# Kernel optimization log

Measured on AMD Instinct MI355X. Metric: run time of the kernel, lower is better.

Reference implementation:

```python
import jax, jax.numpy as jnp
import numpy as np

IN_F, HID, OUT = 128, 128, 32
N_NODES, N_EDGES, N_GRAPHS = 100000, 1600000, 64


def gcn_conv(x, W, b, src, dst, n):
    """PyG-style GCNConv: add self-loops, symmetric deg^-1/2 norm, linear, scatter-add."""
    h = x @ W  # [N, F_out]
    loop = jnp.arange(n)
    src_f = jnp.concatenate([src, loop])
    dst_f = jnp.concatenate([dst, loop])
    deg = jax.ops.segment_sum(jnp.ones_like(dst_f, dtype=x.dtype), dst_f, num_segments=n)
    dinv = jax.lax.rsqrt(jnp.maximum(deg, 1.0))  # deg >= 1 because of self-loops
    norm = dinv[src_f] * dinv[dst_f]             # [E+N]
    msg = h[src_f] * norm[:, None]               # gather + scale, [E+N, F_out]
    out = jax.ops.segment_sum(msg, dst_f, num_segments=n)  # scatter-add
    return out + b


def setup_inputs() -> dict:
    key = jax.random.key(0)
    ks = jax.random.split(key, 10)
    x = jax.random.normal(ks[0], (N_NODES, IN_F), dtype=jnp.float32)
    edge_index = jax.random.randint(ks[1], (2, N_EDGES), 0, N_NODES, dtype=jnp.int64)
    batch = jnp.sort(jax.random.randint(ks[2], (N_NODES,), 0, N_GRAPHS, dtype=jnp.int64))

    def glorot(k, fi, fo):
        s = np.sqrt(6.0 / (fi + fo)).astype(np.float32)
        return jax.random.uniform(k, (fi, fo), dtype=jnp.float32, minval=-s, maxval=s)

    return {
        "x": x,
        "edge_index": edge_index,
        "batch": batch,
        "num_graphs": N_GRAPHS,
        "W1": glorot(ks[3], IN_F, HID), "b1": jnp.zeros((HID,), jnp.float32),
        "W2": glorot(ks[4], HID, HID), "b2": jnp.zeros((HID,), jnp.float32),
        "W3": glorot(ks[5], HID, OUT), "b3": jnp.zeros((OUT,), jnp.float32),
    }


def reference(x, edge_index, batch, num_graphs, W1, b1, W2, b2, W3, b3):
    n = x.shape[0]
    src, dst = edge_index[0], edge_index[1]
    # Dropout is identity in eval mode.
    h = jax.nn.relu(gcn_conv(x, W1, b1, src, dst, n))
    h = jax.nn.relu(gcn_conv(h, W2, b2, src, dst, n))
    h = gcn_conv(h, W3, b3, src, dst, n)  # [N, OUT]
    # global_mean_pool over batch ids
    sums = jax.ops.segment_sum(h, batch, num_segments=num_graphs)
    cnts = jax.ops.segment_sum(jnp.ones((n,), h.dtype), batch, num_segments=num_graphs)
    x_global = sums / jnp.maximum(cnts, 1.0)[:, None]
    return h, x_global
```

## Files before the change

kernel.cpp:

```cpp
#include <hip/hip_runtime.h>
#include <hip/hip_bf16.h>


typedef unsigned int uint32;
typedef short short8 __attribute__((ext_vector_type(8)));
typedef float f32x4 __attribute__((ext_vector_type(4)));

static __device__ __forceinline__ unsigned short f2bf(float f) {
    uint32 u = __float_as_uint(f);
    return (unsigned short)((u + 0x7fffu + ((u >> 16) & 1u)) >> 16);
}
static __device__ __forceinline__ float bf2f_lo(uint32 u) {
    return __uint_as_float(u << 16);
}
static __device__ __forceinline__ float bf2f_hi(uint32 u) {
    return __uint_as_float(u & 0xffff0000u);
}

__global__ __launch_bounds__(256) void initdeg_k(int* deg, int M) {
    int i = blockIdx.x * 256 + threadIdx.x;
    if (i < M) deg[i] = 1;
}

__global__ __launch_bounds__(256) void count_k(const int* __restrict__ dst, int E,
                                               int* __restrict__ deg) {
    int e = blockIdx.x * 256 + threadIdx.x;
    if (e < E) atomicAdd(&deg[dst[e]], 1);
}

__global__ __launch_bounds__(256) void mkdinv_k(const int* __restrict__ deg,
                                                float* __restrict__ dinv, int M) {
    int i = blockIdx.x * 256 + threadIdx.x;
    if (i < M) dinv[i] = rsqrtf((float)deg[i]);
}

__global__ __launch_bounds__(256) void scan1_k(const int* __restrict__ deg, int M,
                                               int* __restrict__ blksum) {
    __shared__ int sh[256];
    int i = blockIdx.x * 256 + threadIdx.x;
    int v = (i < M) ? deg[i] - 1 : 0;
    sh[threadIdx.x] = v;
    __syncthreads();
    for (int o = 128; o > 0; o >>= 1) {
        if (threadIdx.x < o) sh[threadIdx.x] += sh[threadIdx.x + o];
        __syncthreads();
    }
    if (threadIdx.x == 0) blksum[blockIdx.x] = sh[0];
}

__global__ __launch_bounds__(512) void scan2_k(int* __restrict__ blksum, int nb) {
    __shared__ int sh[512];
    int tid = threadIdx.x;
    int v = (tid < nb) ? blksum[tid] : 0;
    sh[tid] = v;
    __syncthreads();
    for (int o = 1; o < 512; o <<= 1) {
        int t = (tid >= o) ? sh[tid - o] : 0;
        __syncthreads();
        sh[tid] += t;
        __syncthreads();
    }
    if (tid < nb) blksum[tid] = sh[tid] - v;
}

__global__ __launch_bounds__(256) void scan3_k(const int* __restrict__ deg, int M,
                                               const int* __restrict__ blksum,
                                               int* __restrict__ rowptr,
                                               int* __restrict__ cursor) {
    __shared__ int sh[256];
    int tid = threadIdx.x;
    int i = blockIdx.x * 256 + tid;
    int v = (i < M) ? deg[i] - 1 : 0;
    sh[tid] = v;
    __syncthreads();
    for (int o = 1; o < 256; o <<= 1) {
        int t = (tid >= o) ? sh[tid - o] : 0;
        __syncthreads();
        sh[tid] += t;
        __syncthreads();
    }
    int excl = sh[tid] - v + blksum[blockIdx.x];
    if (i < M) {
        rowptr[i] = excl;
        cursor[i] = excl;
    }
    if (i == M - 1) rowptr[M] = excl + v;
}

#define FILL_CHUNK 4096
__global__ __launch_bounds__(256) void fill_rp_k(const int* __restrict__ src,
                                                 const int* __restrict__ dst,
                                                 int E, int M,
                                                 int* __restrict__ cursor,
                                                 int* __restrict__ col) {
    const int r = blockIdx.x & 7;
    const int chunk = blockIdx.x >> 3;
    const int lo = (int)(((long long)r * M) >> 3);
    const int hi = (int)(((long long)(r + 1) * M) >> 3);
    const int base = chunk * FILL_CHUNK;
    const int end = min(E, base + FILL_CHUNK);
    for (int e = base + (int)threadIdx.x; e < end; e += 256) {
        int d = dst[e];
        int s = src[e];
        if (d >= lo && d < hi) {
            int slot = atomicAdd(&cursor[d], 1);
            col[slot] = s;
        }
    }
}

__global__ __launch_bounds__(256) void cvt_k(const float* __restrict__ x,
                                             unsigned short* __restrict__ o,
                                             int n8) {
    int i = blockIdx.x * 256 + threadIdx.x;
    if (i >= n8) return;
    const float4* xp = (const float4*)x + (size_t)i * 2;
    float4 a = xp[0], b = xp[1];
    union { unsigned short us[8]; uint4 v; } u;
    u.us[0] = f2bf(a.x); u.us[1] = f2bf(a.y); u.us[2] = f2bf(a.z); u.us[3] = f2bf(a.w);
    u.us[4] = f2bf(b.x); u.us[5] = f2bf(b.y); u.us[6] = f2bf(b.z); u.us[7] = f2bf(b.w);
    *((uint4*)o + i) = u.v;
}

__global__ __launch_bounds__(256) void wt_k(const float* __restrict__ W,
                                            unsigned short* __restrict__ Wt,
                                            int N) {
    int idx = blockIdx.x * 256 + threadIdx.x;
    if (idx >= N * 128) return;
    int n = idx >> 7, k = idx & 127;
    Wt[idx] = f2bf(W[k * N + n]);
}

template <int NT>
__global__ __launch_bounds__(256) void mgemm_k(const unsigned short* __restrict__ A,
                                               const unsigned short* __restrict__ Wt,
                                               unsigned short* __restrict__ C,
                                               int M, int nstrips) {
    constexpr int N = NT * 16;
    const int lane = threadIdx.x & 63;
    const int wid = threadIdx.x >> 6;
    const int r = lane & 15;
    const int g = lane >> 4;

    short8 wf[NT][4];
#pragma unroll
    for (int t = 0; t < NT; t++)
#pragma unroll
        for (int s = 0; s < 4; s++)
            wf[t][s] = *(const short8*)&Wt[(size_t)(t * 16 + r) * 128 + s * 32 + g * 8];

    const int stride = gridDim.x * 4;
    for (int strip = blockIdx.x * 4 + wid; strip < nstrips; strip += stride) {
        const int R = strip * 16;
        const int ar = min(R + r, M - 1);
        short8 af[4];
#pragma unroll
        for (int s = 0; s < 4; s++)
            af[s] = *(const short8*)&A[(size_t)ar * 128 + s * 32 + g * 8];
        f32x4 acc[NT];
#pragma unroll
        for (int t = 0; t < NT; t++) acc[t] = (f32x4){0.f, 0.f, 0.f, 0.f};
#pragma unroll
        for (int s = 0; s < 4; s++)
#pragma unroll
            for (int t = 0; t < NT; t++)
                acc[t] = __builtin_amdgcn_mfma_f32_16x16x32_bf16(
                    af[s], wf[t][s], acc[t], 0, 0, 0);
#pragma unroll
        for (int j = 0; j < 4; j++) {
            int row = R + 4 * g + j;
            if (row < M) {
#pragma unroll
                for (int t = 0; t < NT; t++)
                    C[(size_t)row * N + t * 16 + r] = f2bf(acc[t][j]);
            }
        }
    }
}

__global__ __launch_bounds__(256) void agg128_k(const unsigned short* __restrict__ Hb,
                                                const int* __restrict__ rowptr,
                                                const int* __restrict__ col,
                                                const float* __restrict__ dinv,
                                                const float* __restrict__ bias,
                                                unsigned short* __restrict__ outb,
                                                int M, int relu) {
    int node = blockIdx.x * 4 + (threadIdx.x >> 6);
    if (node >= M) return;
    int lane = threadIdx.x & 63;
    const float di = dinv[node];
    const uint32* Hu = (const uint32*)Hb;
    uint32 su = Hu[(size_t)node * 64 + lane];
    float ax = di * di * bf2f_lo(su);
    float ay = di * di * bf2f_hi(su);
    const int s = rowptr[node], e = rowptr[node + 1];

    for (int base = s; base < e; base += 64) {
        int n = e - base;
        if (n > 64) n = 64;
        int cid = col[base + (lane < n ? lane : 0)];
        float w = di * dinv[cid];
        int j = 0;
        for (; j + 8 <= n; j += 8) {
            int sj[8]; float wj[8]; uint32 u[8];
#pragma unroll
            for (int k = 0; k < 8; k++) {
                sj[k] = __shfl(cid, j + k);
                wj[k] = __shfl(w, j + k);
            }
#pragma unroll
            for (int k = 0; k < 8; k++)
                u[k] = Hu[(size_t)sj[k] * 64 + lane];
#pragma unroll
            for (int k = 0; k < 8; k++) {
                ax = fmaf(wj[k], bf2f_lo(u[k]), ax);
                ay = fmaf(wj[k], bf2f_hi(u[k]), ay);
            }
        }
        for (; j < n; j++) {
            int s0 = __shfl(cid, j);
            float w0 = __shfl(w, j);
            uint32 u0 = Hu[(size_t)s0 * 64 + lane];
            ax = fmaf(w0, bf2f_lo(u0), ax);
            ay = fmaf(w0, bf2f_hi(u0), ay);
        }
    }
    float2 bv = *(const float2*)&bias[lane * 2];
    float ox = ax + bv.x, oy = ay + bv.y;
    if (relu) { ox = fmaxf(ox, 0.f); oy = fmaxf(oy, 0.f); }
    uint32 pk = (uint32)f2bf(ox) | ((uint32)f2bf(oy) << 16);
    *(uint32*)&outb[(size_t)node * 128 + lane * 2] = pk;
}

__global__ __launch_bounds__(256) void agg32_k(const unsigned short* __restrict__ Hb,
                                               const int* __restrict__ rowptr,
                                               const int* __restrict__ col,
                                               const float* __restrict__ dinv,
                                               const float* __restrict__ bias,
                                               float* __restrict__ out, int M) {
    int node = blockIdx.x * 4 + (threadIdx.x >> 6);
    if (node >= M) return;
    int lane = threadIdx.x & 63;
    int f = lane & 31;
    int half = lane >> 5;
    const float di = dinv[node];
    float acc = 0.f;
    if (!half)
        acc = di * di * __uint_as_float(((uint32)Hb[(size_t)node * 32 + f]) << 16);
    const int s = rowptr[node], e = rowptr[node + 1];
    int i = s + half;
    for (; i + 6 < e; i += 8) {
        int s0 = col[i], s1 = col[i + 2], s2 = col[i + 4], s3 = col[i + 6];
        float w0 = di * dinv[s0], w1 = di * dinv[s1];
        float w2 = di * dinv[s2], w3 = di * dinv[s3];
        float h0 = __uint_as_float(((uint32)Hb[(size_t)s0 * 32 + f]) << 16);
        float h1 = __uint_as_float(((uint32)Hb[(size_t)s1 * 32 + f]) << 16);
        float h2 = __uint_as_float(((uint32)Hb[(size_t)s2 * 32 + f]) << 16);
        float h3 = __uint_as_float(((uint32)Hb[(size_t)s3 * 32 + f]) << 16);
        acc = fmaf(w0, h0, acc);
        acc = fmaf(w1, h1, acc);
        acc = fmaf(w2, h2, acc);
        acc = fmaf(w3, h3, acc);
    }
    for (; i < e; i += 2) {
        int s0 = col[i];
        float h0 = __uint_as_float(((uint32)Hb[(size_t)s0 * 32 + f]) << 16);
        acc = fmaf(di * dinv[s0], h0, acc);
    }
    acc += __shfl_xor(acc, 32);
    if (!half) out[(size_t)node * 32 + f] = acc + bias[f];
}

__global__ __launch_bounds__(256) void pool_k(const float* __restrict__ h,
                                              const int* __restrict__ batch, int M,
                                              float* __restrict__ out) {
    int g = blockIdx.x;
    int lo, hi;
    {
        int l = 0, r = M;
        while (l < r) { int m = (l + r) >> 1; if (batch[m] < g) l = m + 1; else r = m; }
        lo = l;
    }
    {
        int l = lo, r = M;
        while (l < r) { int m = (l + r) >> 1; if (batch[m] < g + 1) l = m + 1; else r = m; }
        hi = l;
    }
    int f = threadIdx.x & 31;
    int chunk = threadIdx.x >> 5;
    float acc = 0.f;
    for (int i = lo + chunk; i < hi; i += 8) acc += h[(size_t)i * 32 + f];
    __shared__ float red[8][32];
    red[chunk][f] = acc;
    __syncthreads();
    if (threadIdx.x < 32) {
        float s = 0.f;
#pragma unroll
        for (int c = 0; c < 8; c++) s += red[c][f];
        out[g * 32 + f] = s / fmaxf((float)(hi - lo), 1.f);
    }
}

extern "C" void kernel_launch(void* const* d_in, const int* in_sizes, int n_in,
                              void* d_out, int out_size, void* d_ws, size_t ws_size,
                              hipStream_t stream) {
    const float* x   = (const float*)d_in[0];
    const int* ei    = (const int*)d_in[1];
    const int* batch = (const int*)d_in[2];
    const float* W1  = (const float*)d_in[4];
    const float* b1  = (const float*)d_in[5];
    const float* W2  = (const float*)d_in[6];
    const float* b2  = (const float*)d_in[7];
    const float* W3  = (const float*)d_in[8];
    const float* b3  = (const float*)d_in[9];

    const int M = in_sizes[0] / 128;
    const int E = in_sizes[1] / 2;
    const int G = 64;
    const int* srcp = ei;
    const int* dstp = ei + E;

    char* p = (char*)d_ws;
    auto carve = [&](size_t bytes) {
        void* r = (void*)p;
        p += (bytes + 255) & ~(size_t)255;
        return r;
    };
    int*   deg    = (int*)carve((size_t)M * 4);
    float* dinv   = (float*)carve((size_t)M * 4);
    int*   rowptr = (int*)carve((size_t)(M + 1) * 4);
    int*   cursor = (int*)carve((size_t)M * 4);
    int*   blksum = (int*)carve(512 * 4);
    int*   col    = (int*)carve((size_t)E * 4);
    unsigned short* Xb = (unsigned short*)carve((size_t)M * 128 * 2);
    unsigned short* Hb = (unsigned short*)carve((size_t)M * 128 * 2);
    unsigned short* Ob = (unsigned short*)carve((size_t)M * 128 * 2);
    unsigned short* Wt1 = (unsigned short*)carve(128 * 128 * 2);
    unsigned short* Wt2 = (unsigned short*)carve(128 * 128 * 2);
    unsigned short* Wt3 = (unsigned short*)carve(32 * 128 * 2);

    float* outh = (float*)d_out;
    float* outg = outh + (size_t)M * 32;

    const int nbM = (M + 255) / 256;
    const int nbE = (E + 255) / 256;
    const int nstrips = (M + 15) / 16;
    const int gblk = (nstrips + 7) / 8;

    cvt_k<<<(M * 128 / 8 + 255) / 256, 256, 0, stream>>>(x, Xb, M * 128 / 8);
    initdeg_k<<<nbM, 256, 0, stream>>>(deg, M);
    count_k<<<nbE, 256, 0, stream>>>(dstp, E, deg);
    mkdinv_k<<<nbM, 256, 0, stream>>>(deg, dinv, M);
    scan1_k<<<nbM, 256, 0, stream>>>(deg, M, blksum);
    scan2_k<<<1, 512, 0, stream>>>(blksum, nbM);
    scan3_k<<<nbM, 256, 0, stream>>>(deg, M, blksum, rowptr, cursor);
    {
        const int nchunk = (E + FILL_CHUNK - 1) / FILL_CHUNK;
        fill_rp_k<<<nchunk * 8, 256, 0, stream>>>(srcp, dstp, E, M, cursor, col);
    }
    wt_k<<<(128 * 128 + 255) / 256, 256, 0, stream>>>(W1, Wt1, 128);
    wt_k<<<(128 * 128 + 255) / 256, 256, 0, stream>>>(W2, Wt2, 128);
    wt_k<<<(32 * 128 + 255) / 256, 256, 0, stream>>>(W3, Wt3, 32);

    mgemm_k<8><<<gblk, 256, 0, stream>>>(Xb, Wt1, Hb, M, nstrips);
    agg128_k<<<(M + 3) / 4, 256, 0, stream>>>(Hb, rowptr, col, dinv, b1, Ob, M, 1);
    mgemm_k<8><<<gblk, 256, 0, stream>>>(Ob, Wt2, Hb, M, nstrips);
    agg128_k<<<(M + 3) / 4, 256, 0, stream>>>(Hb, rowptr, col, dinv, b2, Ob, M, 1);
    mgemm_k<2><<<gblk, 256, 0, stream>>>(Ob, Wt3, Hb, M, nstrips);
    agg32_k<<<(M + 3) / 4, 256, 0, stream>>>(Hb, rowptr, col, dinv, b3, outh, M);
    pool_k<<<G, 256, 0, stream>>>(outh, batch, M, outg);
}
```

Baseline: 570.2 us.

## Slice feature layout into 16-wide planes and fold source norm into GEMM

Stores node features as eight 16-column slices (slice-major), so each aggregation block works on one 32-byte slice across many nodes, shrinking the gathered working set per pass for better cache reuse. The source-side deg^-1/2 factor is folded into the GEMM epilogue, which removes the per-edge dinv gather and multiply from the aggregation; the destination factor is applied once per node at the end. Nontemporal hints are added to the streaming edge and column loads. Because gathers become 32-byte rows per slice, sector efficiency depends on how the L2 cache handles the eight slice passes.

```diff
diff --git a/kernel.cpp b/kernel.cpp
--- a/kernel.cpp
+++ b/kernel.cpp
@@ -25,7 +25,7 @@
 __global__ __launch_bounds__(256) void count_k(const int* __restrict__ dst, int E,
                                                int* __restrict__ deg) {
     int e = blockIdx.x * 256 + threadIdx.x;
-    if (e < E) atomicAdd(&deg[dst[e]], 1);
+    if (e < E) atomicAdd(&deg[__builtin_nontemporal_load(&dst[e])], 1);
 }
 
 __global__ __launch_bounds__(256) void mkdinv_k(const int* __restrict__ deg,
@@ -100,8 +100,8 @@
     const int base = chunk * FILL_CHUNK;
     const int end = min(E, base + FILL_CHUNK);
     for (int e = base + (int)threadIdx.x; e < end; e += 256) {
-        int d = dst[e];
-        int s = src[e];
+        int d = __builtin_nontemporal_load(&dst[e]);
+        int s = __builtin_nontemporal_load(&src[e]);
         if (d >= lo && d < hi) {
             int slot = atomicAdd(&cursor[d], 1);
             col[slot] = s;
@@ -111,7 +111,7 @@
 
 __global__ __launch_bounds__(256) void cvt_k(const float* __restrict__ x,
                                              unsigned short* __restrict__ o,
-                                             int n8) {
+                                             int M, int n8) {
     int i = blockIdx.x * 256 + threadIdx.x;
     if (i >= n8) return;
     const float4* xp = (const float4*)x + (size_t)i * 2;
@@ -119,7 +119,10 @@
     union { unsigned short us[8]; uint4 v; } u;
     u.us[0] = f2bf(a.x); u.us[1] = f2bf(a.y); u.us[2] = f2bf(a.z); u.us[3] = f2bf(a.w);
     u.us[4] = f2bf(b.x); u.us[5] = f2bf(b.y); u.us[6] = f2bf(b.z); u.us[7] = f2bf(b.w);
-    *((uint4*)o + i) = u.v;
+    int node = i >> 4;
+    int k0 = (i & 15) * 8;
+    size_t di = ((size_t)(k0 >> 4) * M + node) * 16 + (k0 & 15);
+    *(uint4*)&o[di] = u.v;
 }
 
 __global__ __launch_bounds__(256) void wt_k(const float* __restrict__ W,
@@ -131,9 +134,10 @@
     Wt[idx] = f2bf(W[k * N + n]);
 }
 
-template <int NT>
+template <int NT, bool SOUT>
 __global__ __launch_bounds__(256) void mgemm_k(const unsigned short* __restrict__ A,
                                                const unsigned short* __restrict__ Wt,
+                                               const float* __restrict__ dinv,
                                                unsigned short* __restrict__ C,
                                                int M, int nstrips) {
     constexpr int N = NT * 16;
@@ -155,8 +159,10 @@
         const int ar = min(R + r, M - 1);
         short8 af[4];
 #pragma unroll
-        for (int s = 0; s < 4; s++)
-            af[s] = *(const short8*)&A[(size_t)ar * 128 + s * 32 + g * 8];
+        for (int s = 0; s < 4; s++) {
+            const int q = 2 * s + (g >> 1);
+            af[s] = *(const short8*)&A[((size_t)q * M + ar) * 16 + (g & 1) * 8];
+        }
         f32x4 acc[NT];
 #pragma unroll
         for (int t = 0; t < NT; t++) acc[t] = (f32x4){0.f, 0.f, 0.f, 0.f};
@@ -170,66 +176,70 @@
         for (int j = 0; j < 4; j++) {
             int row = R + 4 * g + j;
             if (row < M) {
-#pragma unroll
-                for (int t = 0; t < NT; t++)
-                    C[(size_t)row * N + t * 16 + r] = f2bf(acc[t][j]);
+                float dv = dinv[row];
+#pragma unroll
+                for (int t = 0; t < NT; t++) {
+                    unsigned short v = f2bf(dv * acc[t][j]);
+                    if (SOUT)
+                        C[((size_t)t * M + row) * 16 + r] = v;
+                    else
+                        C[(size_t)row * N + t * 16 + r] = v;
+                }
             }
         }
     }
 }
 
-__global__ __launch_bounds__(256) void agg128_k(const unsigned short* __restrict__ Hb,
-                                                const int* __restrict__ rowptr,
-                                                const int* __restrict__ col,
-                                                const float* __restrict__ dinv,
-                                                const float* __restrict__ bias,
-                                                unsigned short* __restrict__ outb,
-                                                int M, int relu) {
-    int node = blockIdx.x * 4 + (threadIdx.x >> 6);
+__global__ __launch_bounds__(256) void agg128s_k(const unsigned short* __restrict__ Hs,
+                                                 const int* __restrict__ rowptr,
+                                                 const int* __restrict__ col,
+                                                 const float* __restrict__ dinv,
+                                                 const float* __restrict__ bias,
+                                                 unsigned short* __restrict__ Os,
+                                                 int M, int relu) {
+    const int slice = blockIdx.x & 7;
+    const int nb = blockIdx.x >> 3;
+    const int lane = threadIdx.x & 63;
+    const int wid = threadIdx.x >> 6;
+    const int grp = lane >> 3;
+    const int j = lane & 7;
+    const int node = nb * 32 + wid * 8 + grp;
     if (node >= M) return;
-    int lane = threadIdx.x & 63;
-    const float di = dinv[node];
-    const uint32* Hu = (const uint32*)Hb;
-    uint32 su = Hu[(size_t)node * 64 + lane];
-    float ax = di * di * bf2f_lo(su);
-    float ay = di * di * bf2f_hi(su);
+    const uint32* H = (const uint32*)Hs + (size_t)slice * M * 8;
+    uint32* O = (uint32*)Os + (size_t)slice * M * 8;
+
+    float a0, a1;
+    {
+        uint32 u = H[(size_t)node * 8 + j];
+        a0 = bf2f_lo(u); a1 = bf2f_hi(u);
+    }
     const int s = rowptr[node], e = rowptr[node + 1];
-
-    for (int base = s; base < e; base += 64) {
-        int n = e - base;
-        if (n > 64) n = 64;
-        int cid = col[base + (lane < n ? lane : 0)];
-        float w = di * dinv[cid];
-        int j = 0;
-        for (; j + 8 <= n; j += 8) {
-            int sj[8]; float wj[8]; uint32 u[8];
-#pragma unroll
-            for (int k = 0; k < 8; k++) {
-                sj[k] = __shfl(cid, j + k);
-                wj[k] = __shfl(w, j + k);
-            }
-#pragma unroll
-            for (int k = 0; k < 8; k++)
-                u[k] = Hu[(size_t)sj[k] * 64 + lane];
-#pragma unroll
-            for (int k = 0; k < 8; k++) {
-                ax = fmaf(wj[k], bf2f_lo(u[k]), ax);
-                ay = fmaf(wj[k], bf2f_hi(u[k]), ay);
-            }
-        }
-        for (; j < n; j++) {
-            int s0 = __shfl(cid, j);
-            float w0 = __shfl(w, j);
-            uint32 u0 = Hu[(size_t)s0 * 64 + lane];
-            ax = fmaf(w0, bf2f_lo(u0), ax);
-            ay = fmaf(w0, bf2f_hi(u0), ay);
-        }
-    }
-    float2 bv = *(const float2*)&bias[lane * 2];
-    float ox = ax + bv.x, oy = ay + bv.y;
+    int i = s;
+    for (; i + 4 <= e; i += 4) {
+        int c0 = __builtin_nontemporal_load(&col[i]);
+        int c1 = __builtin_nontemporal_load(&col[i + 1]);
+        int c2 = __builtin_nontemporal_load(&col[i + 2]);
+        int c3 = __builtin_nontemporal_load(&col[i + 3]);
+        uint32 u0 = H[(size_t)c0 * 8 + j];
+        uint32 u1 = H[(size_t)c1 * 8 + j];
+        uint32 u2 = H[(size_t)c2 * 8 + j];
+        uint32 u3 = H[(size_t)c3 * 8 + j];
+        a0 += bf2f_lo(u0); a1 += bf2f_hi(u0);
+        a0 += bf2f_lo(u1); a1 += bf2f_hi(u1);
+        a0 += bf2f_lo(u2); a1 += bf2f_hi(u2);
+        a0 += bf2f_lo(u3); a1 += bf2f_hi(u3);
+    }
+    for (; i < e; i++) {
+        int c0 = __builtin_nontemporal_load(&col[i]);
+        uint32 u0 = H[(size_t)c0 * 8 + j];
+        a0 += bf2f_lo(u0); a1 += bf2f_hi(u0);
+    }
+    float dv = dinv[node];
+    float2 bv = *(const float2*)&bias[slice * 16 + j * 2];
+    float ox = fmaf(dv, a0, bv.x), oy = fmaf(dv, a1, bv.y);
     if (relu) { ox = fmaxf(ox, 0.f); oy = fmaxf(oy, 0.f); }
     uint32 pk = (uint32)f2bf(ox) | ((uint32)f2bf(oy) << 16);
-    *(uint32*)&outb[(size_t)node * 128 + lane * 2] = pk;
+    __builtin_nontemporal_store(pk, &O[(size_t)node * 8 + j]);
 }
 
 __global__ __launch_bounds__(256) void agg32_k(const unsigned short* __restrict__ Hb,
@@ -243,32 +253,28 @@
     int lane = threadIdx.x & 63;
     int f = lane & 31;
     int half = lane >> 5;
-    const float di = dinv[node];
     float acc = 0.f;
     if (!half)
-        acc = di * di * __uint_as_float(((uint32)Hb[(size_t)node * 32 + f]) << 16);
+        acc = __uint_as_float(((uint32)Hb[(size_t)node * 32 + f]) << 16);
     const int s = rowptr[node], e = rowptr[node + 1];
     int i = s + half;
     for (; i + 6 < e; i += 8) {
-        int s0 = col[i], s1 = col[i + 2], s2 = col[i + 4], s3 = col[i + 6];
-        float w0 = di * dinv[s0], w1 = di * dinv[s1];
-        float w2 = di * dinv[s2], w3 = di * dinv[s3];
+        int s0 = __builtin_nontemporal_load(&col[i]);
+        int s1 = __builtin_nontemporal_load(&col[i + 2]);
+        int s2 = __builtin_nontemporal_load(&col[i + 4]);
+        int s3 = __builtin_nontemporal_load(&col[i + 6]);
         float h0 = __uint_as_float(((uint32)Hb[(size_t)s0 * 32 + f]) << 16);
         float h1 = __uint_as_float(((uint32)Hb[(size_t)s1 * 32 + f]) << 16);
         float h2 = __uint_as_float(((uint32)Hb[(size_t)s2 * 32 + f]) << 16);
         float h3 = __uint_as_float(((uint32)Hb[(size_t)s3 * 32 + f]) << 16);
-        acc = fmaf(w0, h0, acc);
-        acc = fmaf(w1, h1, acc);
-        acc = fmaf(w2, h2, acc);
-        acc = fmaf(w3, h3, acc);
+        acc += h0 + h1 + h2 + h3;
     }
     for (; i < e; i += 2) {
-        int s0 = col[i];
-        float h0 = __uint_as_float(((uint32)Hb[(size_t)s0 * 32 + f]) << 16);
-        acc = fmaf(di * dinv[s0], h0, acc);
+        int s0 = __builtin_nontemporal_load(&col[i]);
+        acc += __uint_as_float(((uint32)Hb[(size_t)s0 * 32 + f]) << 16);
     }
     acc += __shfl_xor(acc, 32);
-    if (!half) out[(size_t)node * 32 + f] = acc + bias[f];
+    if (!half) out[(size_t)node * 32 + f] = fmaf(dinv[node], acc, bias[f]);
 }
 
 __global__ __launch_bounds__(256) void pool_k(const float* __restrict__ h,
@@ -332,9 +338,10 @@
     int*   cursor = (int*)carve((size_t)M * 4);
     int*   blksum = (int*)carve(512 * 4);
     int*   col    = (int*)carve((size_t)E * 4);
-    unsigned short* Xb = (unsigned short*)carve((size_t)M * 128 * 2);
-    unsigned short* Hb = (unsigned short*)carve((size_t)M * 128 * 2);
-    unsigned short* Ob = (unsigned short*)carve((size_t)M * 128 * 2);
+    unsigned short* Xs  = (unsigned short*)carve((size_t)M * 128 * 2);
+    unsigned short* Hs  = (unsigned short*)carve((size_t)M * 128 * 2);
+    unsigned short* Os  = (unsigned short*)carve((size_t)M * 128 * 2);
+    unsigned short* H3  = (unsigned short*)carve((size_t)M * 32 * 2);
     unsigned short* Wt1 = (unsigned short*)carve(128 * 128 * 2);
     unsigned short* Wt2 = (unsigned short*)carve(128 * 128 * 2);
     unsigned short* Wt3 = (unsigned short*)carve(32 * 128 * 2);
@@ -346,8 +353,9 @@
     const int nbE = (E + 255) / 256;
     const int nstrips = (M + 15) / 16;
     const int gblk = (nstrips + 7) / 8;
-
-    cvt_k<<<(M * 128 / 8 + 255) / 256, 256, 0, stream>>>(x, Xb, M * 128 / 8);
+    const int ablk = 8 * ((M + 31) / 32);
+
+    cvt_k<<<(M * 128 / 8 + 255) / 256, 256, 0, stream>>>(x, Xs, M, M * 128 / 8);
     initdeg_k<<<nbM, 256, 0, stream>>>(deg, M);
     count_k<<<nbE, 256, 0, stream>>>(dstp, E, deg);
     mkdinv_k<<<nbM, 256, 0, stream>>>(deg, dinv, M);
@@ -362,11 +370,11 @@
     wt_k<<<(128 * 128 + 255) / 256, 256, 0, stream>>>(W2, Wt2, 128);
     wt_k<<<(32 * 128 + 255) / 256, 256, 0, stream>>>(W3, Wt3, 32);
 
-    mgemm_k<8><<<gblk, 256, 0, stream>>>(Xb, Wt1, Hb, M, nstrips);
-    agg128_k<<<(M + 3) / 4, 256, 0, stream>>>(Hb, rowptr, col, dinv, b1, Ob, M, 1);
-    mgemm_k<8><<<gblk, 256, 0, stream>>>(Ob, Wt2, Hb, M, nstrips);
-    agg128_k<<<(M + 3) / 4, 256, 0, stream>>>(Hb, rowptr, col, dinv, b2, Ob, M, 1);
-    mgemm_k<2><<<gblk, 256, 0, stream>>>(Ob, Wt3, Hb, M, nstrips);
-    agg32_k<<<(M + 3) / 4, 256, 0, stream>>>(Hb, rowptr, col, dinv, b3, outh, M);
+    mgemm_k<8, true><<<gblk, 256, 0, stream>>>(Xs, Wt1, dinv, Hs, M, nstrips);
+    agg128s_k<<<ablk, 256, 0, stream>>>(Hs, rowptr, col, dinv, b1, Os, M, 1);
+    mgemm_k<8, true><<<gblk, 256, 0, stream>>>(Os, Wt2, dinv, Hs, M, nstrips);
+    agg128s_k<<<ablk, 256, 0, stream>>>(Hs, rowptr, col, dinv, b2, Os, M, 1);
+    mgemm_k<2, false><<<gblk, 256, 0, stream>>>(Os, Wt3, dinv, H3, M, nstrips);
+    agg32_k<<<(M + 3) / 4, 256, 0, stream>>>(H3, rowptr, col, dinv, b3, outh, M);
     pool_k<<<G, 256, 0, stream>>>(outh, batch, M, outg);
 }
```

Measured after the change: 733.6 us. +28.7%, slower.

## Fold source-side degree norm into GEMM epilogue and drop per-edge dinv gathers

Applied to the files above, without the earlier changes.

The symmetric normalization is factored: the GEMM epilogue scales each output row by dinv[row], so the aggregation kernels only sum neighbor rows and apply dinv[node] once at the end with the bias. This removes the per-edge random dinv gather and the weight shuffles from the inner loops. Edge-index and col reads are marked nontemporal, and the final-layer GEMM output gets its own small buffer. Rounding changes slightly because the scaling happens before the bf16 conversion.

```diff
diff --git a/kernel.cpp b/kernel.cpp
--- a/kernel.cpp
+++ b/kernel.cpp
@@ -25,7 +25,7 @@
 __global__ __launch_bounds__(256) void count_k(const int* __restrict__ dst, int E,
                                                int* __restrict__ deg) {
     int e = blockIdx.x * 256 + threadIdx.x;
-    if (e < E) atomicAdd(&deg[dst[e]], 1);
+    if (e < E) atomicAdd(&deg[__builtin_nontemporal_load(&dst[e])], 1);
 }
 
 __global__ __launch_bounds__(256) void mkdinv_k(const int* __restrict__ deg,
@@ -100,8 +100,8 @@
     const int base = chunk * FILL_CHUNK;
     const int end = min(E, base + FILL_CHUNK);
     for (int e = base + (int)threadIdx.x; e < end; e += 256) {
-        int d = dst[e];
-        int s = src[e];
+        int d = __builtin_nontemporal_load(&dst[e]);
+        int s = __builtin_nontemporal_load(&src[e]);
         if (d >= lo && d < hi) {
             int slot = atomicAdd(&cursor[d], 1);
             col[slot] = s;
@@ -134,6 +134,7 @@
 template <int NT>
 __global__ __launch_bounds__(256) void mgemm_k(const unsigned short* __restrict__ A,
                                                const unsigned short* __restrict__ Wt,
+                                               const float* __restrict__ dinv,
                                                unsigned short* __restrict__ C,
                                                int M, int nstrips) {
     constexpr int N = NT * 16;
@@ -170,9 +171,10 @@
         for (int j = 0; j < 4; j++) {
             int row = R + 4 * g + j;
             if (row < M) {
+                float dv = dinv[row];
 #pragma unroll
                 for (int t = 0; t < NT; t++)
-                    C[(size_t)row * N + t * 16 + r] = f2bf(acc[t][j]);
+                    C[(size_t)row * N + t * 16 + r] = f2bf(dv * acc[t][j]);
             }
         }
     }
@@ -188,45 +190,39 @@
     int node = blockIdx.x * 4 + (threadIdx.x >> 6);
     if (node >= M) return;
     int lane = threadIdx.x & 63;
-    const float di = dinv[node];
     const uint32* Hu = (const uint32*)Hb;
     uint32 su = Hu[(size_t)node * 64 + lane];
-    float ax = di * di * bf2f_lo(su);
-    float ay = di * di * bf2f_hi(su);
+    float ax = bf2f_lo(su);
+    float ay = bf2f_hi(su);
     const int s = rowptr[node], e = rowptr[node + 1];
 
     for (int base = s; base < e; base += 64) {
         int n = e - base;
         if (n > 64) n = 64;
-        int cid = col[base + (lane < n ? lane : 0)];
-        float w = di * dinv[cid];
+        int cid = __builtin_nontemporal_load(&col[base + (lane < n ? lane : 0)]);
         int j = 0;
         for (; j + 8 <= n; j += 8) {
-            int sj[8]; float wj[8]; uint32 u[8];
+            int sj[8]; uint32 u[8];
+#pragma unroll
+            for (int k = 0; k < 8; k++) sj[k] = __shfl(cid, j + k);
+#pragma unroll
+            for (int k = 0; k < 8; k++) u[k] = Hu[(size_t)sj[k] * 64 + lane];
 #pragma unroll
             for (int k = 0; k < 8; k++) {
-                sj[k] = __shfl(cid, j + k);
-                wj[k] = __shfl(w, j + k);
-            }
-#pragma unroll
-            for (int k = 0; k < 8; k++)
-                u[k] = Hu[(size_t)sj[k] * 64 + lane];
-#pragma unroll
-            for (int k = 0; k < 8; k++) {
-                ax = fmaf(wj[k], bf2f_lo(u[k]), ax);
-                ay = fmaf(wj[k], bf2f_hi(u[k]), ay);
+                ax += bf2f_lo(u[k]);
+                ay += bf2f_hi(u[k]);
             }
         }
         for (; j < n; j++) {
             int s0 = __shfl(cid, j);
-            float w0 = __shfl(w, j);
             uint32 u0 = Hu[(size_t)s0 * 64 + lane];
-            ax = fmaf(w0, bf2f_lo(u0), ax);
-            ay = fmaf(w0, bf2f_hi(u0), ay);
+            ax += bf2f_lo(u0);
+            ay += bf2f_hi(u0);
         }
     }
+    float dv = dinv[node];
     float2 bv = *(const float2*)&bias[lane * 2];
-    float ox = ax + bv.x, oy = ay + bv.y;
+    float ox = fmaf(dv, ax, bv.x), oy = fmaf(dv, ay, bv.y);
     if (relu) { ox = fmaxf(ox, 0.f); oy = fmaxf(oy, 0.f); }
     uint32 pk = (uint32)f2bf(ox) | ((uint32)f2bf(oy) << 16);
     *(uint32*)&outb[(size_t)node * 128 + lane * 2] = pk;
@@ -243,32 +239,28 @@
     int lane = threadIdx.x & 63;
     int f = lane & 31;
     int half = lane >> 5;
-    const float di = dinv[node];
     float acc = 0.f;
     if (!half)
-        acc = di * di * __uint_as_float(((uint32)Hb[(size_t)node * 32 + f]) << 16);
+        acc = __uint_as_float(((uint32)Hb[(size_t)node * 32 + f]) << 16);
     const int s = rowptr[node], e = rowptr[node + 1];
     int i = s + half;
     for (; i + 6 < e; i += 8) {
-        int s0 = col[i], s1 = col[i + 2], s2 = col[i + 4], s3 = col[i + 6];
-        float w0 = di * dinv[s0], w1 = di * dinv[s1];
-        float w2 = di * dinv[s2], w3 = di * dinv[s3];
+        int s0 = __builtin_nontemporal_load(&col[i]);
+        int s1 = __builtin_nontemporal_load(&col[i + 2]);
+        int s2 = __builtin_nontemporal_load(&col[i + 4]);
+        int s3 = __builtin_nontemporal_load(&col[i + 6]);
         float h0 = __uint_as_float(((uint32)Hb[(size_t)s0 * 32 + f]) << 16);
         float h1 = __uint_as_float(((uint32)Hb[(size_t)s1 * 32 + f]) << 16);
         float h2 = __uint_as_float(((uint32)Hb[(size_t)s2 * 32 + f]) << 16);
         float h3 = __uint_as_float(((uint32)Hb[(size_t)s3 * 32 + f]) << 16);
-        acc = fmaf(w0, h0, acc);
-        acc = fmaf(w1, h1, acc);
-        acc = fmaf(w2, h2, acc);
-        acc = fmaf(w3, h3, acc);
+        acc += h0 + h1 + h2 + h3;
     }
     for (; i < e; i += 2) {
-        int s0 = col[i];
-        float h0 = __uint_as_float(((uint32)Hb[(size_t)s0 * 32 + f]) << 16);
-        acc = fmaf(di * dinv[s0], h0, acc);
+        int s0 = __builtin_nontemporal_load(&col[i]);
+        acc += __uint_as_float(((uint32)Hb[(size_t)s0 * 32 + f]) << 16);
     }
     acc += __shfl_xor(acc, 32);
-    if (!half) out[(size_t)node * 32 + f] = acc + bias[f];
+    if (!half) out[(size_t)node * 32 + f] = fmaf(dinv[node], acc, bias[f]);
 }
 
 __global__ __launch_bounds__(256) void pool_k(const float* __restrict__ h,
@@ -332,9 +324,10 @@
     int*   cursor = (int*)carve((size_t)M * 4);
     int*   blksum = (int*)carve(512 * 4);
     int*   col    = (int*)carve((size_t)E * 4);
-    unsigned short* Xb = (unsigned short*)carve((size_t)M * 128 * 2);
-    unsigned short* Hb = (unsigned short*)carve((size_t)M * 128 * 2);
-    unsigned short* Ob = (unsigned short*)carve((size_t)M * 128 * 2);
+    unsigned short* Xb  = (unsigned short*)carve((size_t)M * 128 * 2);
+    unsigned short* Hb  = (unsigned short*)carve((size_t)M * 128 * 2);
+    unsigned short* Ob  = (unsigned short*)carve((size_t)M * 128 * 2);
+    unsigned short* H3  = (unsigned short*)carve((size_t)M * 32 * 2);
     unsigned short* Wt1 = (unsigned short*)carve(128 * 128 * 2);
     unsigned short* Wt2 = (unsigned short*)carve(128 * 128 * 2);
     unsigned short* Wt3 = (unsigned short*)carve(32 * 128 * 2);
@@ -362,11 +355,11 @@
     wt_k<<<(128 * 128 + 255) / 256, 256, 0, stream>>>(W2, Wt2, 128);
     wt_k<<<(32 * 128 + 255) / 256, 256, 0, stream>>>(W3, Wt3, 32);
 
-    mgemm_k<8><<<gblk, 256, 0, stream>>>(Xb, Wt1, Hb, M, nstrips);
+    mgemm_k<8><<<gblk, 256, 0, stream>>>(Xb, Wt1, dinv, Hb, M, nstrips);
     agg128_k<<<(M + 3) / 4, 256, 0, stream>>>(Hb, rowptr, col, dinv, b1, Ob, M, 1);
-    mgemm_k<8><<<gblk, 256, 0, stream>>>(Ob, Wt2, Hb, M, nstrips);
+    mgemm_k<8><<<gblk, 256, 0, stream>>>(Ob, Wt2, dinv, Hb, M, nstrips);
     agg128_k<<<(M + 3) / 4, 256, 0, stream>>>(Hb, rowptr, col, dinv, b2, Ob, M, 1);
-    mgemm_k<2><<<gblk, 256, 0, stream>>>(Ob, Wt3, Hb, M, nstrips);
-    agg32_k<<<(M + 3) / 4, 256, 0, stream>>>(Hb, rowptr, col, dinv, b3, outh, M);
+    mgemm_k<2><<<gblk, 256, 0, stream>>>(Ob, Wt3, dinv, H3, M, nstrips);
+    agg32_k<<<(M + 3) / 4, 256, 0, stream>>>(H3, rowptr, col, dinv, b3, outh, M);
     pool_k<<<G, 256, 0, stream>>>(outh, batch, M, outg);
 }
```

Result: slower. 582.3 us (+2.1%).
